# Optimization experiments

Measured on AMD Instinct MI355X. Metric: run time of the kernel, lower is better.

## Reference

```python
import jax, jax.numpy as jnp
import numpy as np

DIM = 256
WH, WW = 7, 7
N = WH * WW
HEADS = 8
HEAD_DIM = DIM // HEADS
SCALE = HEAD_DIM ** -0.5
B_ = 4096
NW = 64  # windows per image; B_ % NW == 0


def _relative_position_index():
    coords = np.stack(np.meshgrid(np.arange(WH), np.arange(WW), indexing='ij'))  # (2,Wh,Ww)
    flat = coords.reshape(2, -1)  # (2,N)
    rel = flat[:, :, None] - flat[:, None, :]  # (2,N,N)
    rel = rel.transpose(1, 2, 0)  # (N,N,2)
    rel = rel + np.array([WH - 1, WW - 1])
    rel = rel * np.array([2 * WW - 1, 1])
    return rel.sum(-1).astype(np.int32)  # (N,N)


def setup_inputs() -> dict:
    key = jax.random.key(0)
    ks = jax.random.split(key, 7)
    num_rel = (2 * WH - 1) * (2 * WW - 1)
    return {
        'x': jax.random.normal(ks[0], (B_, N, DIM), jnp.float32),
        'mask': jax.random.normal(ks[1], (NW, N, N), jnp.float32),
        'qkv_w': jax.random.normal(ks[2], (DIM, 3 * DIM), jnp.float32) * 0.02,
        'qkv_b': jnp.zeros((3 * DIM,), jnp.float32),
        'proj_w': jax.random.normal(ks[3], (DIM, DIM), jnp.float32) * 0.02,
        'proj_b': jnp.zeros((DIM,), jnp.float32),
        'bias_table': jax.random.normal(ks[4], (num_rel, HEADS), jnp.float32) * 0.02,
        'rel_index': jnp.asarray(_relative_position_index()),
    }


def reference(x, mask, qkv_w, qkv_b, proj_w, proj_b, bias_table, rel_index):
    B, n, C = x.shape
    qkv = x @ qkv_w + qkv_b  # (B,N,3C)
    qkv = qkv.reshape(B, n, 3, HEADS, HEAD_DIM).transpose(2, 0, 3, 1, 4)
    q, k, v = qkv[0], qkv[1], qkv[2]  # (B,H,N,hd)
    attn = jnp.einsum('bhnd,bhmd->bhnm', q * SCALE, k)  # (B,H,N,N)
    rel_bias = bias_table[rel_index.reshape(-1)].reshape(n, n, HEADS)
    attn = attn + rel_bias.transpose(2, 0, 1)[None]  # (B,H,N,N)
    nW = mask.shape[0]
    attn = attn.reshape(-1, nW, HEADS, n, n) + mask[None, :, None]
    attn = attn.reshape(-1, HEADS, n, n)
    attn = jax.nn.softmax(attn, axis=-1)
    out = jnp.einsum('bhnm,bhmd->bhnd', attn, v)  # (B,H,N,hd)
    out = out.transpose(0, 2, 1, 3).reshape(B, n, C)
    return out @ proj_w + proj_b
```

## Files before the change

kernel.cpp:

```cpp
#include <hip/hip_runtime.h>
#include <hip/hip_bf16.h>


#define NTOK 49
static constexpr float SCALE_Q = 0.17677669529663687f;

using bf16   = __bf16;
using bf16x4 = __attribute__((ext_vector_type(4))) __bf16;
using bf16x8 = __attribute__((ext_vector_type(8))) __bf16;
using short4v = __attribute__((ext_vector_type(4))) short;
using f32x4  = __attribute__((ext_vector_type(4))) float;

#define WT_QKV_OFF 0
#define WT_PROJ_OFF (768 * 256 * 2)
#define CB_OFF (WT_PROJ_OFF + 256 * 256 * 2)
#define WS_NEEDED (CB_OFF + (size_t)64 * 8 * 4096 * 4)

static __device__ __forceinline__ f32x4 mfma16(bf16x4 a, bf16x4 b, f32x4 c) {
#if __has_builtin(__builtin_amdgcn_mfma_f32_16x16x16_bf16)
    return __builtin_amdgcn_mfma_f32_16x16x16_bf16(a, b, c, 0, 0, 0);
#elif __has_builtin(__builtin_amdgcn_mfma_f32_16x16x16bf16_1k)
    return __builtin_amdgcn_mfma_f32_16x16x16bf16_1k(
        __builtin_bit_cast(short4v, a), __builtin_bit_cast(short4v, b), c, 0, 0, 0);
#elif __has_builtin(__builtin_amdgcn_mfma_f32_16x16x16_bf16_1k)
    return __builtin_amdgcn_mfma_f32_16x16x16_bf16_1k(
        __builtin_bit_cast(short4v, a), __builtin_bit_cast(short4v, b), c, 0, 0, 0);
#else
    asm volatile("v_mfma_f32_16x16x16_bf16 %0, %1, %2, %0\n\t"
                 "s_nop 7\n\ts_nop 7\n\ts_nop 1"
                 : "+v"(c) : "v"(a), "v"(b));
    return c;
#endif
}

__global__ void prep_wqkv(const float* __restrict__ qkv_w, bf16* __restrict__ wt) {
    int idx = blockIdx.x * 256 + threadIdx.x;
    if (idx >= 768 * 256) return;
    int n = idx >> 8, k = idx & 255;
    float v = qkv_w[k * 768 + n];
    if (n < 256) v *= SCALE_Q;
    wt[idx] = (bf16)v;
}
__global__ void prep_wproj(const float* __restrict__ proj_w, bf16* __restrict__ wt) {
    int idx = blockIdx.x * 256 + threadIdx.x;
    if (idx >= 256 * 256) return;
    int n = idx >> 8, k = idx & 255;
    wt[idx] = (bf16)proj_w[k * 256 + n];
}
__global__ void prep_cb2(const float* __restrict__ bias_table, const int* __restrict__ rel_index,
                         const float* __restrict__ mask, float* __restrict__ cb2) {
    int idx = blockIdx.x * 256 + threadIdx.x;
    if (idx >= 64 * 8 * 4096) return;
    int r    = idx & 3;
    int lane = (idx >> 2) & 63;
    int qp   = (idx >> 8) & 15;
    int h    = (idx >> 12) & 7;
    int w    = idx >> 15;
    int kt = qp >> 2, qt = qp & 3;
    int i = qt * 16 + (lane & 15);
    int j = kt * 16 + (lane >> 4) * 4 + r;
    float v;
    if (j >= NTOK)      v = -1e30f;
    else if (i >= NTOK) v = 0.0f;
    else v = bias_table[rel_index[i * 49 + j] * 8 + h] + mask[(w * 49 + i) * 49 + j];
    cb2[idx] = v;
}

__global__ __launch_bounds__(512, 2) void fused_attn(
    const float* __restrict__ x,
    const float* __restrict__ qkv_b,
    const float* __restrict__ proj_b,
    const bf16* __restrict__ wt_qkv,
    const bf16* __restrict__ wt_proj,
    const float* __restrict__ cb2,
    float* __restrict__ out)
{
    __shared__ char xs[32768];
    const int b    = blockIdx.x;
    const int tid  = threadIdx.x;
    const int lane = tid & 63;
    const int h    = tid >> 6;
    const int c    = lane & 15;
    const int g    = lane >> 4;

    {
        const float* xb = x + (size_t)b * (NTOK * 256);
        #pragma unroll
        for (int it = 0; it < 8; ++it) {
            int idx = it * 512 + tid;
            int row = idx >> 6, c4 = idx & 63;
            float4 v = make_float4(0.f, 0.f, 0.f, 0.f);
            if (row < NTOK) v = ((const float4*)xb)[row * 64 + c4];
            bf16x4 o;
            o[0] = (bf16)v.x; o[1] = (bf16)v.y; o[2] = (bf16)v.z; o[3] = (bf16)v.w;
            *(bf16x4*)(xs + row * 512 + ((c4 * 8) ^ ((row & 7) << 4))) = o;
        }
    }
    __syncthreads();

    bf16x4 iden;
    #pragma unroll
    for (int j = 0; j < 4; ++j) iden[j] = (bf16)((4 * g + j == c) ? 1.0f : 0.0f);

    bf16x4 qf[4][2];
    bf16x4 kf[4][2];
    bf16x4 vf[2][4];

    {
        f32x4 acc[6][4];
        #pragma unroll
        for (int ni = 0; ni < 6; ++ni)
            #pragma unroll
            for (int mi = 0; mi < 4; ++mi)
                acc[ni][mi] = (f32x4){0.f, 0.f, 0.f, 0.f};

        __builtin_amdgcn_s_setprio(1);
        #pragma unroll
        for (int kk = 0; kk < 8; ++kk) {
            bf16x8 a[4];
            #pragma unroll
            for (int mi = 0; mi < 4; ++mi) {
                int row = mi * 16 + c;
                a[mi] = *(const bf16x8*)(xs + row * 512 + ((kk * 64 + g * 16) ^ ((row & 7) << 4)));
            }
            #pragma unroll
            for (int ni = 0; ni < 6; ++ni) {
                int ncol = (ni >> 1) * 256 + h * 32 + (ni & 1) * 16 + c;
                bf16x8 bfr = *(const bf16x8*)(wt_qkv + ncol * 256 + kk * 32 + g * 8);
                #pragma unroll
                for (int mi = 0; mi < 4; ++mi)
                    acc[ni][mi] = __builtin_amdgcn_mfma_f32_16x16x32_bf16(a[mi], bfr, acc[ni][mi], 0, 0, 0);
            }
        }
        __builtin_amdgcn_s_setprio(0);

        #pragma unroll
        for (int ni = 0; ni < 6; ++ni) {
            int col = (ni >> 1) * 256 + h * 32 + (ni & 1) * 16 + c;
            float bias = qkv_b[col];
            if (ni < 2) bias *= SCALE_Q;
            #pragma unroll
            for (int mi = 0; mi < 4; ++mi) {
                bf16x4 in;
                #pragma unroll
                for (int r = 0; r < 4; ++r) in[r] = (bf16)(acc[ni][mi][r] + bias);
                if (ni < 4) {
                    f32x4 t = mfma16(in, iden, (f32x4){0.f, 0.f, 0.f, 0.f});
                    bf16x4 o;
                    #pragma unroll
                    for (int r = 0; r < 4; ++r) o[r] = (bf16)t[r];
                    if (ni < 2) qf[mi][ni] = o;
                    else        kf[mi][ni - 2] = o;
                } else {
                    vf[ni - 4][mi] = in;
                }
            }
        }
    }
    __syncthreads();

    const float* cbw = cb2 + ((size_t)((b & 63) * 8 + h)) * 4096;
    #pragma unroll
    for (int qt = 0; qt < 4; ++qt) {
        f32x4 cbv[4];
        #pragma unroll
        for (int kt = 0; kt < 4; ++kt)
            cbv[kt] = *(const f32x4*)(cbw + (kt * 4 + qt) * 256 + lane * 4);

        f32x4 sT[4];
        __builtin_amdgcn_s_setprio(1);
        #pragma unroll
        for (int kt = 0; kt < 4; ++kt) {
            sT[kt] = (f32x4){0.f, 0.f, 0.f, 0.f};
            sT[kt] = mfma16(kf[kt][0], qf[qt][0], sT[kt]);
            sT[kt] = mfma16(kf[kt][1], qf[qt][1], sT[kt]);
        }
        __builtin_amdgcn_s_setprio(0);
        #pragma unroll
        for (int kt = 0; kt < 4; ++kt)
            #pragma unroll
            for (int r = 0; r < 4; ++r)
                sT[kt][r] += cbv[kt][r];
        float m = sT[0][0];
        #pragma unroll
        for (int kt = 0; kt < 4; ++kt)
            #pragma unroll
            for (int r = 0; r < 4; ++r) m = fmaxf(m, sT[kt][r]);
        m = fmaxf(m, __shfl_xor(m, 16));
        m = fmaxf(m, __shfl_xor(m, 32));
        float sum = 0.f;
        #pragma unroll
        for (int kt = 0; kt < 4; ++kt)
            #pragma unroll
            for (int r = 0; r < 4; ++r) {
                float e = __expf(sT[kt][r] - m);
                sT[kt][r] = e;
                sum += e;
            }
        sum += __shfl_xor(sum, 16);
        sum += __shfl_xor(sum, 32);
        float rs = 1.f / sum;
        bf16x4 pB[4];
        #pragma unroll
        for (int kt = 0; kt < 4; ++kt)
            #pragma unroll
            for (int r = 0; r < 4; ++r) pB[kt][r] = (bf16)(sT[kt][r] * rs);
        __builtin_amdgcn_s_setprio(1);
        #pragma unroll
        for (int dt = 0; dt < 2; ++dt) {
            f32x4 oT = (f32x4){0.f, 0.f, 0.f, 0.f};
            #pragma unroll
            for (int kt = 0; kt < 4; ++kt)
                oT = mfma16(vf[dt][kt], pB[kt], oT);
            int row = qt * 16 + c;
            int cbyte = h * 64 + dt * 32 + g * 8;
            bf16x4 o;
            #pragma unroll
            for (int r = 0; r < 4; ++r) o[r] = (bf16)oT[r];
            *(bf16x4*)(xs + row * 512 + (cbyte ^ ((row & 7) << 4))) = o;
        }
        __builtin_amdgcn_s_setprio(0);
    }
    __syncthreads();

    {
        f32x4 po[2][4];
        #pragma unroll
        for (int ni = 0; ni < 2; ++ni)
            #pragma unroll
            for (int mi = 0; mi < 4; ++mi)
                po[ni][mi] = (f32x4){0.f, 0.f, 0.f, 0.f};

        __builtin_amdgcn_s_setprio(1);
        #pragma unroll
        for (int kk = 0; kk < 8; ++kk) {
            bf16x8 a[4];
            #pragma unroll
            for (int mi = 0; mi < 4; ++mi) {
                int row = mi * 16 + c;
                a[mi] = *(const bf16x8*)(xs + row * 512 + ((kk * 64 + g * 16) ^ ((row & 7) << 4)));
            }
            #pragma unroll
            for (int ni = 0; ni < 2; ++ni) {
                int col = h * 32 + ni * 16 + c;
                bf16x8 bw = *(const bf16x8*)(wt_proj + col * 256 + kk * 32 + g * 8);
                #pragma unroll
                for (int mi = 0; mi < 4; ++mi)
                    po[ni][mi] = __builtin_amdgcn_mfma_f32_16x16x32_bf16(a[mi], bw, po[ni][mi], 0, 0, 0);
            }
        }
        __builtin_amdgcn_s_setprio(0);
        float* outb = out + (size_t)b * (NTOK * 256);
        #pragma unroll
        for (int ni = 0; ni < 2; ++ni) {
            int col = h * 32 + ni * 16 + c;
            float pb = proj_b[col];
            #pragma unroll
            for (int mi = 0; mi < 4; ++mi) {
                #pragma unroll
                for (int r = 0; r < 4; ++r) {
                    int row = mi * 16 + g * 4 + r;
                    if (row < NTOK) outb[row * 256 + col] = po[ni][mi][r] + pb;
                }
            }
        }
    }
}

extern "C" void kernel_launch(void* const* d_in, const int* in_sizes, int n_in,
                              void* d_out, int out_size, void* d_ws, size_t ws_size,
                              hipStream_t stream) {
    const float* x          = (const float*)d_in[0];
    const float* mask       = (const float*)d_in[1];
    const float* qkv_w      = (const float*)d_in[2];
    const float* qkv_b      = (const float*)d_in[3];
    const float* proj_w     = (const float*)d_in[4];
    const float* proj_b     = (const float*)d_in[5];
    const float* bias_table = (const float*)d_in[6];
    const int*   rel_index  = (const int*)d_in[7];
    float* out = (float*)d_out;

    if (ws_size < WS_NEEDED) return;

    char* ws = (char*)d_ws;
    bf16*  wt_qkv  = (bf16*)(ws + WT_QKV_OFF);
    bf16*  wt_proj = (bf16*)(ws + WT_PROJ_OFF);
    float* cb2     = (float*)(ws + CB_OFF);

    prep_wqkv <<<768, 256, 0, stream>>>(qkv_w, wt_qkv);
    prep_wproj<<<256, 256, 0, stream>>>(proj_w, wt_proj);
    prep_cb2  <<<(64 * 8 * 4096 + 255) / 256, 256, 0, stream>>>(bias_table, rel_index, mask, cb2);

    fused_attn<<<4096, 512, 0, stream>>>(x, qkv_b, proj_b, wt_qkv, wt_proj, cb2, out);
}
```

Baseline: 424.8 us.

## Split combined bias+mask table into per-head bias and per-window mask staged in LDS

Replaces the precomputed 64x8 combined relative-bias-plus-mask table (8 MB) with a small per-head bias table and a per-window mask table. Each block stages its window's mask into shared memory once and shares it across all 8 heads, while the bias table is small and cache-resident. This cuts the prep kernel's write traffic and the main kernel's global reads of the bias tensor. In exchange, shared memory per block grows from 32 KB to 48 KB, which may limit occupancy at 2 blocks per CU, and there is one extra add per score element.

```diff
diff --git a/kernel.cpp b/kernel.cpp
--- a/kernel.cpp
+++ b/kernel.cpp
@@ -13,8 +13,9 @@
 
 #define WT_QKV_OFF 0
 #define WT_PROJ_OFF (768 * 256 * 2)
-#define CB_OFF (WT_PROJ_OFF + 256 * 256 * 2)
-#define WS_NEEDED (CB_OFF + (size_t)64 * 8 * 4096 * 4)
+#define SB_OFF (WT_PROJ_OFF + 256 * 256 * 2)
+#define SM_OFF (SB_OFF + 8 * 4096 * 4)
+#define WS_NEEDED (SM_OFF + (size_t)64 * 4096 * 4)
 
 static __device__ __forceinline__ f32x4 mfma16(bf16x4 a, bf16x4 b, f32x4 c) {
 #if __has_builtin(__builtin_amdgcn_mfma_f32_16x16x16_bf16)
@@ -47,23 +48,34 @@
     int n = idx >> 8, k = idx & 255;
     wt[idx] = (bf16)proj_w[k * 256 + n];
 }
-__global__ void prep_cb2(const float* __restrict__ bias_table, const int* __restrict__ rel_index,
-                         const float* __restrict__ mask, float* __restrict__ cb2) {
+__global__ void prep_sb(const float* __restrict__ bias_table, const int* __restrict__ rel_index,
+                        float* __restrict__ sb) {
     int idx = blockIdx.x * 256 + threadIdx.x;
-    if (idx >= 64 * 8 * 4096) return;
+    if (idx >= 8 * 4096) return;
     int r    = idx & 3;
     int lane = (idx >> 2) & 63;
     int qp   = (idx >> 8) & 15;
-    int h    = (idx >> 12) & 7;
-    int w    = idx >> 15;
+    int h    = idx >> 12;
     int kt = qp >> 2, qt = qp & 3;
     int i = qt * 16 + (lane & 15);
     int j = kt * 16 + (lane >> 4) * 4 + r;
     float v;
     if (j >= NTOK)      v = -1e30f;
     else if (i >= NTOK) v = 0.0f;
-    else v = bias_table[rel_index[i * 49 + j] * 8 + h] + mask[(w * 49 + i) * 49 + j];
-    cb2[idx] = v;
+    else v = bias_table[rel_index[i * 49 + j] * 8 + h];
+    sb[idx] = v;
+}
+__global__ void prep_sm(const float* __restrict__ mask, float* __restrict__ sm) {
+    int idx = blockIdx.x * 256 + threadIdx.x;
+    if (idx >= 64 * 4096) return;
+    int r    = idx & 3;
+    int lane = (idx >> 2) & 63;
+    int qp   = (idx >> 8) & 15;
+    int w    = idx >> 12;
+    int kt = qp >> 2, qt = qp & 3;
+    int i = qt * 16 + (lane & 15);
+    int j = kt * 16 + (lane >> 4) * 4 + r;
+    sm[idx] = (i < NTOK && j < NTOK) ? mask[(w * 49 + i) * 49 + j] : 0.0f;
 }
 
 __global__ __launch_bounds__(512, 2) void fused_attn(
@@ -72,10 +84,13 @@
     const float* __restrict__ proj_b,
     const bf16* __restrict__ wt_qkv,
     const bf16* __restrict__ wt_proj,
-    const float* __restrict__ cb2,
+    const float* __restrict__ sb,
+    const float* __restrict__ sm,
     float* __restrict__ out)
 {
-    __shared__ char xs[32768];
+    __shared__ char smem[49152];
+    char* xs  = smem;
+    char* smL = smem + 32768;
     const int b    = blockIdx.x;
     const int tid  = threadIdx.x;
     const int lane = tid & 63;
@@ -94,6 +109,12 @@
             bf16x4 o;
             o[0] = (bf16)v.x; o[1] = (bf16)v.y; o[2] = (bf16)v.z; o[3] = (bf16)v.w;
             *(bf16x4*)(xs + row * 512 + ((c4 * 8) ^ ((row & 7) << 4))) = o;
+        }
+        const float4* smw = (const float4*)(sm + (size_t)(b & 63) * 4096);
+        #pragma unroll
+        for (int t = 0; t < 2; ++t) {
+            int off = t * 512 + tid;
+            *(float4*)(smL + off * 16) = smw[off];
         }
     }
     __syncthreads();
@@ -159,13 +180,16 @@
     }
     __syncthreads();
 
-    const float* cbw = cb2 + ((size_t)((b & 63) * 8 + h)) * 4096;
+    const float* sbh = sb + (size_t)h * 4096;
     #pragma unroll
     for (int qt = 0; qt < 4; ++qt) {
-        f32x4 cbv[4];
-        #pragma unroll
-        for (int kt = 0; kt < 4; ++kt)
-            cbv[kt] = *(const f32x4*)(cbw + (kt * 4 + qt) * 256 + lane * 4);
+        f32x4 sbv[4], smv[4];
+        #pragma unroll
+        for (int kt = 0; kt < 4; ++kt)
+            sbv[kt] = *(const f32x4*)(sbh + (kt * 4 + qt) * 256 + lane * 4);
+        #pragma unroll
+        for (int kt = 0; kt < 4; ++kt)
+            smv[kt] = *(const f32x4*)(smL + ((kt * 4 + qt) * 64 + lane) * 16);
 
         f32x4 sT[4];
         __builtin_amdgcn_s_setprio(1);
@@ -180,7 +204,7 @@
         for (int kt = 0; kt < 4; ++kt)
             #pragma unroll
             for (int r = 0; r < 4; ++r)
-                sT[kt][r] += cbv[kt][r];
+                sT[kt][r] += sbv[kt][r] + smv[kt][r];
         float m = sT[0][0];
         #pragma unroll
         for (int kt = 0; kt < 4; ++kt)
@@ -285,11 +309,13 @@
     char* ws = (char*)d_ws;
     bf16*  wt_qkv  = (bf16*)(ws + WT_QKV_OFF);
     bf16*  wt_proj = (bf16*)(ws + WT_PROJ_OFF);
-    float* cb2     = (float*)(ws + CB_OFF);
+    float* sbp     = (float*)(ws + SB_OFF);
+    float* smp     = (float*)(ws + SM_OFF);
 
     prep_wqkv <<<768, 256, 0, stream>>>(qkv_w, wt_qkv);
     prep_wproj<<<256, 256, 0, stream>>>(proj_w, wt_proj);
-    prep_cb2  <<<(64 * 8 * 4096 + 255) / 256, 256, 0, stream>>>(bias_table, rel_index, mask, cb2);
-
-    fused_attn<<<4096, 512, 0, stream>>>(x, qkv_b, proj_b, wt_qkv, wt_proj, cb2, out);
-}
+    prep_sb   <<<128, 256, 0, stream>>>(bias_table, rel_index, sbp);
+    prep_sm   <<<1024, 256, 0, stream>>>(mask, smp);
+
+    fused_attn<<<4096, 512, 0, stream>>>(x, qkv_b, proj_b, wt_qkv, wt_proj, sbp, smp, out);
+}
```

Result: no change. 424.5 us (-0.1%).
